# Kernel tuning notes

Measured on AMD Instinct MI355X. Metric: run time of the kernel, lower is better.

Reference implementation:

```python
import jax, jax.numpy as jnp
import numpy as np

B, N, D, DFC, EMB, L = 16, 1024, 128, 128, 64, 4
NHOPS = (1, 2, 3, 4)  # tatic='cont': nhop(i) = i + 1
EDGE_P = 0.03


def _make_adj(k):
    u = jax.random.uniform(k, (B, N, N))
    a = u < EDGE_P
    a = a | jnp.transpose(a, (0, 2, 1))          # undirected
    a = a | jnp.eye(N, dtype=bool)[None]         # self loops
    return a.astype(jnp.float32)


def setup_inputs() -> dict:
    key = jax.random.key(0)
    ks = jax.random.split(key, 16)
    s = 0.05
    x = jax.random.normal(ks[0], (B, N, 2 * EMB), jnp.float32)
    adj1 = _make_adj(ks[1])
    adj2 = _make_adj(ks[2])
    valid = jnp.ones((B, N), jnp.float32)
    embede_w = jax.random.normal(ks[3], (D, 2 * EMB)) * s
    gW = jax.random.normal(ks[4], (L, D, D)) * s
    gb = jnp.zeros((L, D), jnp.float32)
    gA = jax.random.normal(ks[5], (L, D, D)) * s
    gate_w = jax.random.normal(ks[6], (L, 1, 2 * D)) * s
    gate_b = jnp.zeros((L, 1), jnp.float32)
    fc0_w = jax.random.normal(ks[7], (DFC, D)) * s
    fc0_b = jnp.zeros((DFC,), jnp.float32)
    fc1_w = jax.random.normal(ks[8], (DFC, DFC)) * s
    fc1_b = jnp.zeros((DFC,), jnp.float32)
    fc2_w = jax.random.normal(ks[9], (DFC, DFC)) * s
    fc2_b = jnp.zeros((DFC,), jnp.float32)
    fc3_w = jax.random.normal(ks[10], (1, DFC)) * s
    fc3_b = jnp.zeros((1,), jnp.float32)
    return dict(x=x, adj1=adj1, adj2=adj2, valid=valid, embede_w=embede_w,
                gW=gW, gb=gb, gA=gA, gate_w=gate_w, gate_b=gate_b,
                fc0_w=fc0_w, fc0_b=fc0_b, fc1_w=fc1_w, fc1_b=fc1_b,
                fc2_w=fc2_w, fc2_b=fc2_b, fc3_w=fc3_w, fc3_b=fc3_b)


def _glema(x, adj, W, b, A, gw, gbias, nhop):
    h = x @ W.T + b                                        # [B,N,D]
    e = jnp.einsum('bjl,bkl->bjk', jnp.einsum('bjd,de->bje', h, A), h)
    e = e + jnp.transpose(e, (0, 2, 1))                    # undirected
    att = jnp.where(adj > 0, e, jnp.float32(0.0))
    att = jax.nn.softmax(att, axis=1) * adj                # softmax over dim 1, then adj mask
    az = jax.nn.relu(jnp.einsum('bij,bjd->bid', att, h))
    coeff = jax.nn.sigmoid(jnp.concatenate([h, az], -1) @ gw.T + gbias)  # [B,N,1]
    z = h
    for _ in range(nhop):
        az = jax.nn.relu(jnp.einsum('bij,bjd->bid', att, z))
        z = coeff * h + (1.0 - coeff) * az
    return z


def reference(x, adj1, adj2, valid, embede_w, gW, gb, gA, gate_w, gate_b,
              fc0_w, fc0_b, fc1_w, fc1_b, fc2_w, fc2_b, fc3_w, fc3_b):
    h = x @ embede_w.T                                     # embede (no bias)
    for k in range(L):                                     # branch='both': c_hs2 - c_hs1
        h1 = _glema(h, adj1, gW[k], gb[k], gA[k], gate_w[k], gate_b[k], NHOPS[k])
        h2 = _glema(h, adj2, gW[k], gb[k], gA[k], gate_w[k], gate_b[k], NHOPS[k])
        h = h2 - h1                                        # dropout p used in eval mode -> identity
    h = h * valid[..., None]
    pooled = h.sum(1) / valid.sum(1, keepdims=True)        # [B,D]
    y = jax.nn.relu(pooled @ fc0_w.T + fc0_b)
    y = jax.nn.relu(y @ fc1_w.T + fc1_b)
    y = jax.nn.relu(y @ fc2_w.T + fc2_b)
    y = jax.nn.sigmoid(y @ fc3_w.T + fc3_b)
    return y.reshape(-1)                                   # [B]
```

## Files before the change

kernel.cpp:

```cpp
#include <hip/hip_runtime.h>

typedef _Float16 half_t;
typedef _Float16 half8 __attribute__((ext_vector_type(8)));
typedef _Float16 half4v __attribute__((ext_vector_type(4)));
typedef float floatx4 __attribute__((ext_vector_type(4)));

#define MFMA(a,b,c) __builtin_amdgcn_mfma_f32_16x16x32_f16(a,b,c,0,0,0)

#define NB 16
#define NLEN 1024
#define DD 128
#define BN (NB*NLEN)
#define BND ((size_t)NB*NLEN*DD)
#define BNN ((size_t)NB*NLEN*NLEN)
#define ELLS 128
#define EMP 1044

static __device__ inline float f16lo(unsigned pk) {
    unsigned short us = (unsigned short)(pk & 0xffffu);
    half_t h; __builtin_memcpy(&h, &us, 2); return (float)h;
}

__global__ __launch_bounds__(256)
void k_embed(const float* __restrict__ x, const float* __restrict__ Ew, half_t* __restrict__ h16) {
    __shared__ float rows[8][DD];
    int g = blockIdx.x * 8;
    int tid = threadIdx.x;
    {
        int nl = tid >> 5, c4 = (tid & 31) * 4;
        *(float4*)&rows[nl][c4] = *(const float4*)&x[(size_t)(g + nl) * DD + c4];
    }
    __syncthreads();
    int t = tid & 127, half = tid >> 7;
    const float* wr = Ew + (size_t)t * DD;
    float acc[4] = {0.f, 0.f, 0.f, 0.f};
    for (int k = 0; k < DD; k++) {
        float w = wr[k];
#pragma unroll
        for (int m = 0; m < 4; m++) acc[m] += rows[half + 2 * m][k] * w;
    }
#pragma unroll
    for (int m = 0; m < 4; m++) h16[(size_t)(g + half + 2 * m) * DD + t] = (half_t)acc[m];
}

__global__ __launch_bounds__(256)
void k_adjmask(const float* __restrict__ adj, unsigned int* __restrict__ mask) {
    int widx = blockIdx.x * 256 + threadIdx.x;
    const float* p = adj + (size_t)widx * 32;
    unsigned int m = 0;
#pragma unroll
    for (int i = 0; i < 32; i += 4) {
        float4 v = *(const float4*)&p[i];
        m |= (v.x > 0.f ? 1u : 0u) << i;
        m |= (v.y > 0.f ? 1u : 0u) << (i + 1);
        m |= (v.z > 0.f ? 1u : 0u) << (i + 2);
        m |= (v.w > 0.f ? 1u : 0u) << (i + 3);
    }
    mask[widx] = m;
}

__global__ __launch_bounds__(256)
void k_ell(const unsigned* __restrict__ mask1, const unsigned* __restrict__ mask2,
           unsigned* __restrict__ ell, unsigned* __restrict__ cntA) {
    int t = threadIdx.x, w = t >> 6, l = t & 63;
    int R = blockIdx.x * 4 + w;
    int br = R >> 14, nb = R & 16383;
    const unsigned* mg = br ? mask2 : mask1;
    unsigned m = (l < 32) ? mg[(size_t)nb * 32 + l] : 0u;
    int c = __popc(m);
    int P = c;
    for (int off = 1; off < 64; off <<= 1) {
        int u = __shfl_up(P, off);
        if (l >= off) P += u;
    }
    int excl = P - c;
    int total = __shfl(P, 31);
    if (total > ELLS) total = ELLS;
    if (l == 0) cntA[R] = (unsigned)total;
    unsigned mm = m; int off = excl;
    while (mm) {
        int b2 = __ffs(mm) - 1; mm &= mm - 1;
        if (off < ELLS) ell[(size_t)R * ELLS + off] = ((unsigned)(l * 32 + b2)) << 16;
        off++;
    }
    for (int s = total + l; s < ELLS; s += 64) ell[(size_t)R * ELLS + s] = 0u;
}

__global__ __launch_bounds__(256)
void k_wcast(const float* __restrict__ gW, const float* __restrict__ gA,
             half_t* __restrict__ Wf, half_t* __restrict__ STf) {
    int i = blockIdx.x * 256 + threadIdx.x;
    Wf[i] = (half_t)gW[i];
    int base = i & ~16383;
    int lrem = i & 16383;
    int d = lrem >> 7, e = lrem & 127;
    STf[base + (e << 7) + d] = (half_t)(gA[i] + gA[base + (e << 7) + d]);
}

__global__ __launch_bounds__(256)
void k_proj(const half_t* __restrict__ pa, const half_t* __restrict__ pb,
            const half_t* __restrict__ Wf, const float* __restrict__ bias,
            const half_t* __restrict__ STf,
            half_t* __restrict__ hbr16, half_t* __restrict__ hbrF, half_t* __restrict__ hSF) {
    __shared__ half_t htile[32 * 136];
    __shared__ half_t hbtile[32 * 136];
    int g = blockIdx.x * 32;
    int t = threadIdx.x;
    int w = t >> 6, l = t & 63, q = l >> 4, l15 = l & 15;
#pragma unroll
    for (int v = 0; v < 2; v++) {
        int idx = v * 256 + t; int r = idx >> 4, c8 = (idx & 15) * 8;
        half8 va = *(const half8*)&pa[((size_t)(g + r) << 7) + c8];
        if (pb) {
            half8 vb = *(const half8*)&pb[((size_t)(g + r) << 7) + c8];
            va = va - vb;
        }
        *(half8*)&htile[r * 136 + c8] = va;
    }
    __syncthreads();
    int rowh = (w & 1) * 16;
    int c0 = (w >> 1) * 4;
    half8 a1[4];
#pragma unroll
    for (int kc = 0; kc < 4; kc++) a1[kc] = *(const half8*)&htile[(rowh + l15) * 136 + kc * 32 + q * 8];
    floatx4 acc[4];
#pragma unroll
    for (int cc = 0; cc < 4; cc++) {
        int col = (c0 + cc) * 16 + l15;
        floatx4 a = {0.f, 0.f, 0.f, 0.f};
#pragma unroll
        for (int kc = 0; kc < 4; kc++) {
            half8 bf = *(const half8*)&Wf[((size_t)col << 7) + kc * 32 + q * 8];
            a = MFMA(a1[kc], bf, a);
        }
        float bv = bias[col];
        a.x += bv; a.y += bv; a.z += bv; a.w += bv;
        acc[cc] = a;
    }
#pragma unroll
    for (int cc = 0; cc < 4; cc++) {
        int col = (c0 + cc) * 16 + l15;
#pragma unroll
        for (int r = 0; r < 4; r++)
            hbtile[(rowh + q * 4 + r) * 136 + col] = (half_t)acc[cc][r];
    }
    __syncthreads();
    half8 a2[4];
#pragma unroll
    for (int kc = 0; kc < 4; kc++) a2[kc] = *(const half8*)&hbtile[(rowh + l15) * 136 + kc * 32 + q * 8];
#pragma unroll
    for (int cc = 0; cc < 4; cc++) {
        int col = (c0 + cc) * 16 + l15;
        floatx4 a = {0.f, 0.f, 0.f, 0.f};
#pragma unroll
        for (int kc = 0; kc < 4; kc++) {
            half8 bf = *(const half8*)&STf[((size_t)col << 7) + kc * 32 + q * 8];
            a = MFMA(a2[kc], bf, a);
        }
        acc[cc] = a;
    }
    __syncthreads();
#pragma unroll
    for (int cc = 0; cc < 4; cc++) {
        int col = (c0 + cc) * 16 + l15;
#pragma unroll
        for (int r = 0; r < 4; r++) htile[(rowh + q * 4 + r) * 136 + col] = (half_t)acc[cc][r];
    }
    __syncthreads();
#pragma unroll
    for (int v = 0; v < 2; v++) {
        int idx = v * 256 + t; int r = idx >> 4, c8 = (idx & 15) * 8;
        *(half8*)&hbr16[((size_t)(g + r) << 7) + c8] = *(const half8*)&hbtile[r * 136 + c8];
    }
#pragma unroll
    for (int v = 0; v < 2; v++) {
        int fi = v * 256 + t;
        int g2 = fi >> 8, kc = (fi >> 6) & 3, li = fi & 63;
        int src = (g2 * 16 + (li & 15)) * 136 + kc * 32 + (li >> 4) * 8;
        size_t dst = (((size_t)(blockIdx.x * 2 + g2) * 4 + kc) << 10) + li * 8;
        *(half8*)&hbrF[dst] = *(const half8*)&hbtile[src];
        *(half8*)&hSF[dst]  = *(const half8*)&htile[src];
    }
}

__global__ __launch_bounds__(256)
void k_E(const half_t* __restrict__ hSF, const half_t* __restrict__ hbrF,
         const half_t* __restrict__ hbr16,
         unsigned* __restrict__ ell, const unsigned* __restrict__ cntA,
         float* __restrict__ rsr, half_t* __restrict__ hbrs) {
    int b = blockIdx.y, s = blockIdx.x;
    int t = threadIdx.x, w = t >> 6, l = t & 63, q = l >> 4, l15 = l & 15;
    __shared__ half_t emS[16 * EMP];
    __shared__ float rsS[2][16];
    size_t Gb = (size_t)b * 64;
    half8 A[4];
#pragma unroll
    for (int kc = 0; kc < 4; kc++)
        A[kc] = *(const half8*)&hSF[(((Gb + s) * 4 + kc) << 10) + l * 8];
#pragma unroll 4
    for (int cg = 0; cg < 16; cg++) {
        int c0 = w * 256 + cg * 16;
        floatx4 a = {0.f, 0.f, 0.f, 0.f};
#pragma unroll
        for (int kc = 0; kc < 4; kc++) {
            half8 bf = *(const half8*)&hbrF[(((Gb + w * 16 + cg) * 4 + kc) << 10) + l * 8];
            a = MFMA(A[kc], bf, a);
        }
#pragma unroll
        for (int r = 0; r < 4; r++)
            emS[(q * 4 + r) * EMP + c0 + l15] = (half_t)a[r];
    }
    __syncthreads();
    const float CN = 0.000335462627903f;
#pragma unroll
    for (int rr = 0; rr < 4; rr++) {
        int rl = w * 4 + rr;
        int rowg = b * 1024 + s * 16 + rl;
#pragma unroll
        for (int br = 0; br < 2; br++) {
            size_t R = ((size_t)br << 14) + rowg;
            int cn = (int)cntA[R];
            float rs = 0.f;
            for (int base = 0; base < cn; base += 64) {
                int si = base + l;
                float v = 0.f;
                if (si < cn) {
                    unsigned pk = ell[R * ELLS + si];
                    int col = (int)(pk >> 16);
                    float em = (float)emS[rl * EMP + col];
                    v = __expf(em - 8.f);
                    half_t hv = (half_t)v;
                    unsigned short us; __builtin_memcpy(&us, &hv, 2);
                    ((unsigned short*)ell)[(R * ELLS + si) * 2] = us;
                }
                rs += v;
            }
            rs += __shfl_xor(rs, 1); rs += __shfl_xor(rs, 2);
            rs += __shfl_xor(rs, 4); rs += __shfl_xor(rs, 8);
            rs += __shfl_xor(rs, 16); rs += __shfl_xor(rs, 32);
            if (l == 0) {
                float rv = 1.f / (rs + (1024.f - (float)cn) * CN);
                rsr[R] = rv;
                rsS[br][rl] = rv;
            }
        }
    }
    __syncthreads();
    const half_t* hrow = hbr16 + ((size_t)b << 17) + ((size_t)(s * 16) << 7);
#pragma unroll
    for (int v = 0; v < 2; v++) {
        int idx = v * 256 + t;
        int row = idx >> 5, br2 = (idx >> 4) & 1, ch = idx & 15;
        half8 hv = *(const half8*)&hrow[(size_t)row * 128 + ch * 8];
        float sc = rsS[br2][row];
        half8 o;
#pragma unroll
        for (int d = 0; d < 8; d++) o[d] = (half_t)(sc * (float)hv[d]);
        *(half8*)&hbrs[(size_t)br2 * BND + ((size_t)(b * 1024 + s * 16 + row) << 7) + ch * 8] = o;
    }
}

__global__ __launch_bounds__(256)
void k_az(const unsigned* __restrict__ ell, const unsigned* __restrict__ cntA,
          const float* __restrict__ rsr,
          const half_t* __restrict__ zin, const half_t* __restrict__ hbr16,
          const float* __restrict__ gw, const float* __restrict__ gb_,
          float* __restrict__ cfb, half_t* __restrict__ outp, int mode) {
    int t = threadIdx.x, w = t >> 6, l = t & 63;
    int g = l >> 4, l15 = l & 15;
    int R = blockIdx.x * 16 + w * 4 + g;
    int br = R >> 14, nb = R & 16383;
    const unsigned* ep = ell + (size_t)R * ELLS;
    int cn = (int)cntA[R];
    const half_t* zb = zin + (size_t)br * BND + (((size_t)(nb & ~1023)) << 7) + l15 * 8;
    float acc[8] = {};
    for (int s = 0; s < cn; s += 4) {
        uint4 p4 = *(const uint4*)(ep + s);
        unsigned pk[4] = {p4.x, p4.y, p4.z, p4.w};
#pragma unroll
        for (int i = 0; i < 4; i++) {
            half8 zz = *(const half8*)(zb + (((size_t)(pk[i] >> 16)) << 7));
            float v = f16lo(pk[i]);
#pragma unroll
            for (int d = 0; d < 8; d++) acc[d] += v * (float)zz[d];
        }
    }
#pragma unroll
    for (int d = 0; d < 8; d++) acc[d] = fmaxf(acc[d], 0.f);
    half8 hv8 = *(const half8*)&hbr16[((size_t)nb << 7) + l15 * 8];
    float hv[8];
#pragma unroll
    for (int d = 0; d < 8; d++) hv[d] = (float)hv8[d];
    float cf;
    if (mode >= 3) {
        const float* g1 = gw + l15 * 8;
        const float* g2 = gw + 128 + l15 * 8;
        float dp = 0.f;
#pragma unroll
        for (int d = 0; d < 8; d++) dp += hv[d] * g1[d] + acc[d] * g2[d];
        dp += __shfl_xor(dp, 1); dp += __shfl_xor(dp, 2);
        dp += __shfl_xor(dp, 4); dp += __shfl_xor(dp, 8);
        cf = 1.f / (1.f + __expf(-(dp + gb_[0])));
        if (l15 == 0) cfb[R] = cf;
    } else {
        cf = cfb[R];
    }
    float sc = (mode == 1 || mode == 3) ? rsr[R] : 1.f;
    half8 o;
#pragma unroll
    for (int d = 0; d < 8; d++)
        o[d] = (half_t)(sc * (cf * hv[d] + (1.f - cf) * acc[d]));
    *(half8*)&outp[(size_t)R * DD + l15 * 8] = o;
}

__global__ __launch_bounds__(256)
void k_pool(const half_t* __restrict__ z2, const half_t* __restrict__ z1,
            const float* __restrict__ valid, float* __restrict__ part) {
    int b = blockIdx.y, s = blockIdx.x;
    int t = threadIdx.x, d = t & 127, hf = t >> 7;
    __shared__ float red[128];
    float acc = 0.f;
    int nbase = s * 128 + hf * 64;
    for (int n = nbase; n < nbase + 64; n++) {
        size_t gi = ((size_t)(b * 1024 + n) << 7) + d;
        acc += ((float)z2[gi] - (float)z1[gi]) * valid[b * 1024 + n];
    }
    if (hf) red[d] = acc;
    __syncthreads();
    if (!hf) part[(b * 8 + s) * 128 + d] = acc + red[d];
}

__global__ __launch_bounds__(128)
void k_mlp(const float* __restrict__ part, const float* __restrict__ valid,
           const float* __restrict__ w0, const float* __restrict__ b0,
           const float* __restrict__ w1, const float* __restrict__ b1,
           const float* __restrict__ w2, const float* __restrict__ b2,
           const float* __restrict__ w3, const float* __restrict__ b3,
           float* __restrict__ out) {
    int b = blockIdx.x, t = threadIdx.x;
    __shared__ float y0[DD], y1[DD];
    __shared__ float sred[2];
    float vs = 0.f;
    for (int n = t; n < NLEN; n += 128) vs += valid[b * NLEN + n];
    for (int off = 32; off; off >>= 1) vs += __shfl_down(vs, off);
    if ((t & 63) == 0) sred[t >> 6] = vs;
    __syncthreads();
    float vsum = sred[0] + sred[1];
    float acc = 0.f;
#pragma unroll
    for (int s = 0; s < 8; s++) acc += part[(b * 8 + s) * 128 + t];
    y0[t] = acc / vsum;
    __syncthreads();
    float a = b0[t];
    for (int k = 0; k < DD; k++) a += y0[k] * w0[t * DD + k];
    y1[t] = fmaxf(a, 0.f);
    __syncthreads();
    a = b1[t];
    for (int k = 0; k < DD; k++) a += y1[k] * w1[t * DD + k];
    y0[t] = fmaxf(a, 0.f);
    __syncthreads();
    a = b2[t];
    for (int k = 0; k < DD; k++) a += y0[k] * w2[t * DD + k];
    y1[t] = fmaxf(a, 0.f);
    __syncthreads();
    float p = y1[t] * w3[t];
    for (int off = 32; off; off >>= 1) p += __shfl_down(p, off);
    if ((t & 63) == 0) sred[t >> 6] = p;
    __syncthreads();
    if (t == 0) out[b] = 1.f / (1.f + __expf(-(sred[0] + sred[1] + b3[0])));
}

extern "C" void kernel_launch(void* const* d_in, const int* in_sizes, int n_in,
                              void* d_out, int out_size, void* d_ws, size_t ws_size,
                              hipStream_t stream) {
    (void)in_sizes; (void)n_in; (void)out_size; (void)ws_size;
    const float* x     = (const float*)d_in[0];
    const float* adj1  = (const float*)d_in[1];
    const float* adj2  = (const float*)d_in[2];
    const float* valid = (const float*)d_in[3];
    const float* Ew    = (const float*)d_in[4];
    const float* gW    = (const float*)d_in[5];
    const float* gb    = (const float*)d_in[6];
    const float* gA    = (const float*)d_in[7];
    const float* gatew = (const float*)d_in[8];
    const float* gateb = (const float*)d_in[9];
    const float* w0 = (const float*)d_in[10]; const float* b0 = (const float*)d_in[11];
    const float* w1 = (const float*)d_in[12]; const float* b1 = (const float*)d_in[13];
    const float* w2 = (const float*)d_in[14]; const float* b2 = (const float*)d_in[15];
    const float* w3 = (const float*)d_in[16]; const float* b3 = (const float*)d_in[17];
    float* out = (float*)d_out;

    char* p = (char*)d_ws;
    float* rsr  = (float*)p; p += 2 * BN * 4;
    float* cfb  = (float*)p; p += 2 * BN * 4;
    float* partb = (float*)p; p += (size_t)NB * 8 * 128 * 4;
    half_t* h16   = (half_t*)p; p += BND * 2;
    half_t* hbr16 = (half_t*)p; p += BND * 2;
    half_t* hbrF  = (half_t*)p; p += BND * 2;
    half_t* hSF   = (half_t*)p; p += BND * 2;
    half_t* hbrs  = (half_t*)p; p += 2 * BND * 2;
    half_t* zf    = (half_t*)p; p += 2 * BND * 2;
    half_t* zsA   = (half_t*)p; p += 2 * BND * 2;
    half_t* zsB   = (half_t*)p; p += 2 * BND * 2;
    unsigned* ell = (unsigned*)p; p += (size_t)2 * BN * ELLS * 4;
    unsigned* cntA = (unsigned*)p; p += (size_t)2 * BN * 4;
    unsigned* mask1 = (unsigned*)p; p += (BNN / 32) * 4;
    unsigned* mask2 = (unsigned*)p; p += (BNN / 32) * 4;
    half_t* Wf16 = (half_t*)p; p += (size_t)4 * 128 * 128 * 2;
    half_t* ST16 = (half_t*)p; p += (size_t)4 * 128 * 128 * 2;

    k_wcast<<<256, 256, 0, stream>>>(gW, gA, Wf16, ST16);
    k_adjmask<<<2048, 256, 0, stream>>>(adj1, mask1);
    k_adjmask<<<2048, 256, 0, stream>>>(adj2, mask2);
    k_ell<<<8192, 256, 0, stream>>>(mask1, mask2, ell, cntA);
    k_embed<<<2048, 256, 0, stream>>>(x, Ew, h16);

    for (int k = 0; k < 4; k++) {
        int nhop = k + 1;
        const half_t* pa = k ? (zf + BND) : h16;
        const half_t* pb = k ? zf : nullptr;
        k_proj<<<512, 256, 0, stream>>>(pa, pb, Wf16 + (size_t)k * 16384, gb + k * 128,
                                        ST16 + (size_t)k * 16384, hbr16, hbrF, hSF);
        k_E<<<dim3(64, NB), 256, 0, stream>>>(hSF, hbrF, hbr16, ell, cntA, rsr, hbrs);
        half_t* tgate = (nhop == 1) ? zf : zsA;
        k_az<<<2048, 256, 0, stream>>>(ell, cntA, rsr, hbrs, hbr16,
                                       gatew + k * 256, gateb + k, cfb, tgate,
                                       (nhop == 1) ? 4 : 3);
        half_t* src = tgate;
        for (int hop = 2; hop <= nhop; hop++) {
            half_t* dst = (hop == nhop) ? zf : ((hop & 1) ? zsA : zsB);
            k_az<<<2048, 256, 0, stream>>>(ell, cntA, rsr, src, hbr16,
                                           gatew + k * 256, gateb + k, cfb, dst,
                                           (hop == nhop) ? 2 : 1);
            src = dst;
        }
    }
    k_pool<<<dim3(8, NB), 256, 0, stream>>>(zf + BND, zf, valid, partb);
    k_mlp<<<16, 128, 0, stream>>>(partb, valid, w0, b0, w1, b1, w2, b2, w3, b3, out);
}
```

Before: 722.8 us.

## Fuse preprocessing kernels and accumulate sparse aggregation in packed fp16

Result: faster. 699.2 us (-3.3%).

```diff
diff --git a/kernel.cpp b/kernel.cpp
--- a/kernel.cpp
+++ b/kernel.cpp
@@ -20,12 +20,27 @@
     unsigned short us = (unsigned short)(pk & 0xffffu);
     half_t h; __builtin_memcpy(&h, &us, 2); return (float)h;
 }
-
-__global__ __launch_bounds__(256)
-void k_embed(const float* __restrict__ x, const float* __restrict__ Ew, half_t* __restrict__ h16) {
+static __device__ inline half_t f16h(unsigned pk) {
+    unsigned short us = (unsigned short)(pk & 0xffffu);
+    half_t h; __builtin_memcpy(&h, &us, 2); return h;
+}
+
+__global__ __launch_bounds__(256)
+void k_prep(const float* __restrict__ x, const float* __restrict__ Ew, half_t* __restrict__ h16,
+            const float* __restrict__ gW, const float* __restrict__ gA,
+            half_t* __restrict__ Wf, half_t* __restrict__ STf) {
+    int tid = threadIdx.x;
+    if (blockIdx.x >= 2048) {
+        int i = (blockIdx.x - 2048) * 256 + tid;
+        Wf[i] = (half_t)gW[i];
+        int base = i & ~16383;
+        int lrem = i & 16383;
+        int d = lrem >> 7, e = lrem & 127;
+        STf[base + (e << 7) + d] = (half_t)(gA[i] + gA[base + (e << 7) + d]);
+        return;
+    }
     __shared__ float rows[8][DD];
     int g = blockIdx.x * 8;
-    int tid = threadIdx.x;
     {
         int nl = tid >> 5, c4 = (tid & 31) * 4;
         *(float4*)&rows[nl][c4] = *(const float4*)&x[(size_t)(g + nl) * DD + c4];
@@ -44,57 +59,39 @@
 }
 
 __global__ __launch_bounds__(256)
-void k_adjmask(const float* __restrict__ adj, unsigned int* __restrict__ mask) {
-    int widx = blockIdx.x * 256 + threadIdx.x;
-    const float* p = adj + (size_t)widx * 32;
-    unsigned int m = 0;
+void k_ell(const float* __restrict__ adj1, const float* __restrict__ adj2,
+           unsigned* __restrict__ ell, unsigned* __restrict__ cntA) {
+    int t = threadIdx.x, w = t >> 6, l = t & 63;
+    int half = l >> 5, l32 = l & 31;
+    int R = blockIdx.x * 8 + w * 2 + half;
+    int br = R >> 14, nb = R & 16383;
+    const float* arow = (br ? adj2 : adj1) + (size_t)nb * 1024 + l32 * 32;
+    unsigned m = 0;
 #pragma unroll
     for (int i = 0; i < 32; i += 4) {
-        float4 v = *(const float4*)&p[i];
+        float4 v = *(const float4*)&arow[i];
         m |= (v.x > 0.f ? 1u : 0u) << i;
         m |= (v.y > 0.f ? 1u : 0u) << (i + 1);
         m |= (v.z > 0.f ? 1u : 0u) << (i + 2);
         m |= (v.w > 0.f ? 1u : 0u) << (i + 3);
     }
-    mask[widx] = m;
-}
-
-__global__ __launch_bounds__(256)
-void k_ell(const unsigned* __restrict__ mask1, const unsigned* __restrict__ mask2,
-           unsigned* __restrict__ ell, unsigned* __restrict__ cntA) {
-    int t = threadIdx.x, w = t >> 6, l = t & 63;
-    int R = blockIdx.x * 4 + w;
-    int br = R >> 14, nb = R & 16383;
-    const unsigned* mg = br ? mask2 : mask1;
-    unsigned m = (l < 32) ? mg[(size_t)nb * 32 + l] : 0u;
     int c = __popc(m);
     int P = c;
-    for (int off = 1; off < 64; off <<= 1) {
-        int u = __shfl_up(P, off);
-        if (l >= off) P += u;
+    for (int off = 1; off < 32; off <<= 1) {
+        int u = __shfl_up(P, off, 32);
+        if (l32 >= off) P += u;
     }
     int excl = P - c;
-    int total = __shfl(P, 31);
+    int total = __shfl(P, 31, 32);
     if (total > ELLS) total = ELLS;
-    if (l == 0) cntA[R] = (unsigned)total;
+    if (l32 == 0) cntA[R] = (unsigned)total;
     unsigned mm = m; int off = excl;
     while (mm) {
         int b2 = __ffs(mm) - 1; mm &= mm - 1;
-        if (off < ELLS) ell[(size_t)R * ELLS + off] = ((unsigned)(l * 32 + b2)) << 16;
+        if (off < ELLS) ell[(size_t)R * ELLS + off] = ((unsigned)(l32 * 32 + b2)) << 16;
         off++;
     }
-    for (int s = total + l; s < ELLS; s += 64) ell[(size_t)R * ELLS + s] = 0u;
-}
-
-__global__ __launch_bounds__(256)
-void k_wcast(const float* __restrict__ gW, const float* __restrict__ gA,
-             half_t* __restrict__ Wf, half_t* __restrict__ STf) {
-    int i = blockIdx.x * 256 + threadIdx.x;
-    Wf[i] = (half_t)gW[i];
-    int base = i & ~16383;
-    int lrem = i & 16383;
-    int d = lrem >> 7, e = lrem & 127;
-    STf[base + (e << 7) + d] = (half_t)(gA[i] + gA[base + (e << 7) + d]);
+    for (int s = total + l32; s < ELLS; s += 32) ell[(size_t)R * ELLS + s] = 0u;
 }
 
 __global__ __launch_bounds__(256)
@@ -273,20 +270,21 @@
     const unsigned* ep = ell + (size_t)R * ELLS;
     int cn = (int)cntA[R];
     const half_t* zb = zin + (size_t)br * BND + (((size_t)(nb & ~1023)) << 7) + l15 * 8;
-    float acc[8] = {};
+    half8 acc8 = {};
     for (int s = 0; s < cn; s += 4) {
         uint4 p4 = *(const uint4*)(ep + s);
         unsigned pk[4] = {p4.x, p4.y, p4.z, p4.w};
 #pragma unroll
         for (int i = 0; i < 4; i++) {
             half8 zz = *(const half8*)(zb + (((size_t)(pk[i] >> 16)) << 7));
-            float v = f16lo(pk[i]);
-#pragma unroll
-            for (int d = 0; d < 8; d++) acc[d] += v * (float)zz[d];
-        }
-    }
-#pragma unroll
-    for (int d = 0; d < 8; d++) acc[d] = fmaxf(acc[d], 0.f);
+            half_t hv = f16h(pk[i]);
+            half8 vv = {hv, hv, hv, hv, hv, hv, hv, hv};
+            acc8 += zz * vv;
+        }
+    }
+    float acc[8];
+#pragma unroll
+    for (int d = 0; d < 8; d++) acc[d] = fmaxf((float)acc8[d], 0.f);
     half8 hv8 = *(const half8*)&hbr16[((size_t)nb << 7) + l15 * 8];
     float hv[8];
 #pragma unroll
@@ -404,16 +402,11 @@
     half_t* zsB   = (half_t*)p; p += 2 * BND * 2;
     unsigned* ell = (unsigned*)p; p += (size_t)2 * BN * ELLS * 4;
     unsigned* cntA = (unsigned*)p; p += (size_t)2 * BN * 4;
-    unsigned* mask1 = (unsigned*)p; p += (BNN / 32) * 4;
-    unsigned* mask2 = (unsigned*)p; p += (BNN / 32) * 4;
     half_t* Wf16 = (half_t*)p; p += (size_t)4 * 128 * 128 * 2;
     half_t* ST16 = (half_t*)p; p += (size_t)4 * 128 * 128 * 2;
 
-    k_wcast<<<256, 256, 0, stream>>>(gW, gA, Wf16, ST16);
-    k_adjmask<<<2048, 256, 0, stream>>>(adj1, mask1);
-    k_adjmask<<<2048, 256, 0, stream>>>(adj2, mask2);
-    k_ell<<<8192, 256, 0, stream>>>(mask1, mask2, ell, cntA);
-    k_embed<<<2048, 256, 0, stream>>>(x, Ew, h16);
+    k_prep<<<2304, 256, 0, stream>>>(x, Ew, h16, gW, gA, Wf16, ST16);
+    k_ell<<<4096, 256, 0, stream>>>(adj1, adj2, ell, cntA);
 
     for (int k = 0; k < 4; k++) {
         int nhop = k + 1;
```
